# Kernel tuning notes

Hardware: AMD Instinct MI355X
Metric: run time of the kernel (lower is better)

The kernel has to match this reference:

```python
import jax, jax.numpy as jnp
import numpy as np

B, F, D = 2048, 40, 32
CIN = (64, 64)


def _glorot(key, shape):
    fan_in, fan_out = shape[1] * shape[2], shape[0] * shape[2]
    std = jnp.sqrt(2.0 / (fan_in + fan_out)).astype(jnp.float32)
    return jax.random.normal(key, shape, dtype=jnp.float32) * std


def setup_inputs() -> dict:
    key = jax.random.key(0)
    kx, k0, k1 = jax.random.split(key, 3)
    x = jax.random.normal(kx, (B, F, D), dtype=jnp.float32)
    W0 = _glorot(k0, (CIN[0], F * F, D))
    b0 = jnp.zeros((CIN[0],), dtype=jnp.float32)
    W1 = _glorot(k1, (CIN[1], F * CIN[0], D))
    b1 = jnp.zeros((CIN[1],), dtype=jnp.float32)
    return {"x": x, "W0": W0, "b0": b0, "W1": W1, "b1": b1}


def _cin_step(x0, xk, W, b):
    # x0: (B,F,D)  xk: (B,H,D)  W: (O, H*F, D)  b: (O,)
    Bn, H, Dn = xk.shape
    Fn = x0.shape[1]
    # outer product per embedding channel, h-major flatten as in tf.reshape
    z = jnp.einsum('bhd,bfd->bhfd', xk, x0).reshape(Bn, H * Fn, Dn)
    # per-embedding-channel contraction against weights: (B,D,O)
    y = jnp.einsum('bhd,ohd->bdo', z, W) + b
    y = jax.nn.relu(y)
    return jnp.transpose(y, (0, 2, 1))  # (B,O,D)


def reference(x, W0, b0, W1, b1):
    x1 = _cin_step(x, x, W0, b0)
    x2 = _cin_step(x, x1, W1, b1)
    final = jnp.concatenate([x, x1, x2], axis=1)  # (B, F+O0+O1, D)
    return jnp.sum(final, axis=-1)  # (B, F+O0+O1)
```

## Files before the change

### kernel.cpp

```cpp
#include <hip/hip_runtime.h>

typedef unsigned int   u32;
typedef unsigned short u16;
typedef _Float16       f16;

using f16x8  = __attribute__((ext_vector_type(8)))  _Float16;
using f16x4  = __attribute__((ext_vector_type(4)))  _Float16;
using f32x16 = __attribute__((ext_vector_type(16))) float;

#define LLDS16(G, L) __builtin_amdgcn_global_load_lds( \
  (const __attribute__((address_space(1))) u32*)(G), \
  (__attribute__((address_space(3))) u32*)(L), 16, 0, 0)

#define WAITV(N) { asm volatile("s_waitcnt vmcnt(" #N ")" ::: "memory"); \
                   __builtin_amdgcn_sched_barrier(0); }
#define FENCE_BAR() { asm volatile("s_waitcnt lgkmcnt(0)" ::: "memory"); \
                      __builtin_amdgcn_sched_barrier(0); \
                      __builtin_amdgcn_s_barrier(); \
                      __builtin_amdgcn_sched_barrier(0); }
#define BAR() { __builtin_amdgcn_s_barrier(); __builtin_amdgcn_sched_barrier(0); }
#define KEEP(x) asm volatile("" : "+v"(x))

__global__ __launch_bounds__(256)
void prep(const float* __restrict__ x,
          const float* __restrict__ W0, const float* __restrict__ W1,
          f16* __restrict__ xt, f16* __restrict__ W0p, f16* __restrict__ W1p,
          float* __restrict__ out){
  __shared__ char shm[33920];
  const int tid = threadIdx.x;
  if (blockIdx.x < 2560){
    float (*tile)[33] = (float(*)[33])shm;
    const int r0 = blockIdx.x << 5;
    const int c  = tid & 31;
    const int rp = tid >> 5;
#pragma unroll
    for (int p = 0; p < 4; ++p){
      const int r = (p << 3) + rp;
      float v = x[(size_t)(r0 + r) * 32 + c];
      tile[r][c] = v;
      float s = v;
#pragma unroll
      for (int off = 16; off > 0; off >>= 1) s += __shfl_xor(s, off, 32);
      if (c == 0){
        const int row = r0 + r;
        out[(size_t)(row / 40) * 168 + (row % 40)] = s;
      }
    }
    __syncthreads();
#pragma unroll
    for (int p = 0; p < 4; ++p){
      const int dd = (p << 3) + rp;
      xt[(size_t)dd * 81920 + r0 + c] = (f16)tile[c][dd];
    }
  } else {
    u16* t = (u16*)shm;
    int kb = blockIdx.x - 2560;
    const float* in; f16* outp; int K;
    if (kb < 200){ in = W0; outp = W0p; K = 1600; }
    else         { kb -= 200; in = W1; outp = W1p; K = 2560; }
    const int kbase = kb << 3;
#pragma unroll 4
    for (int i = 0; i < 64; ++i){
      const int idx = tid + (i << 8);
      const int o   = idx >> 8;
      const int rem = idx & 255;
      const int e   = rem >> 5;
      const int dd  = rem & 31;
      const float v = in[(size_t)o * (K * 32) + (size_t)(kbase + e) * 32 + dd];
      union { f16 h; u16 u; } cv; cv.h = (f16)v;
      t[dd * 530 + o * 8 + e] = cv.u;
    }
    __syncthreads();
    const u32* t32 = (const u32*)t;
    u32* o32 = (u32*)outp;
    const int obase = kb << 8;
#pragma unroll 4
    for (int i = 0; i < 32; ++i){
      const int idx = tid + (i << 8);
      const int dd  = idx >> 8;
      const int rem = idx & 255;
      o32[(size_t)dd * (K * 32) + obase + rem] = t32[dd * 265 + rem];
    }
  }
}

__global__ __launch_bounds__(256, 2)
void cin_fused(const f16* __restrict__ xt,
               const f16* __restrict__ W0p,
               const f16* __restrict__ W1p,
               const float* __restrict__ b0v, const float* __restrict__ b1v,
               f16* __restrict__ x1s,
               f16* __restrict__ y2s){
  constexpr int X0OFF = 40960;
  constexpr int X1OFF = 53248;
  constexpr int X0MS  = 32 * 96;
  constexpr int X1MS  = 32 * 144;

  const int bid = blockIdx.x;
  const int d   = ((bid & 7) << 2) | ((bid >> 3) & 3);
  const int b0  = (bid >> 5) << 7;
  const int tid = threadIdx.x;
  const int wv  = tid >> 6;
  const int wr  = wv >> 1;
  const int wc  = wv & 1;
  const int l   = tid & 63;
  const int hi  = l >> 5;
  const int lr  = l & 31;

  __shared__ char smem[71680];

  const f16* gW0 = W0p + (size_t)d * 102400;
  const f16* gW1 = W1p + (size_t)d * 163840;

#define ISSUE(I) do { \
    const f16* src_ = ((I) < 10) ? (gW0 + (size_t)(I) * 10240) \
                                 : (gW1 + (size_t)((I) - 10) * 10240); \
    const f16* gt_ = src_ + wv * 2560 + l * 8; \
    char* lb_ = smem + ((I) & 1) * 20480 + wv * 5120; \
    _Pragma("unroll") \
    for (int j_ = 0; j_ < 5; ++j_) LLDS16(gt_ + j_ * 512, lb_ + j_ * 1024); \
  } while (0)

  ISSUE(0);
  ISSUE(1);

  {
    const uint4* src = (const uint4*)(xt + (size_t)d * 81920 + (size_t)b0 * 40);
#pragma unroll
    for (int it = 0; it < 3; ++it){
      const int idx = tid + (it << 8);
      if (idx < 640){
        const int r = idx / 5, c = idx - r * 5;
        *(uint4*)(smem + X0OFF + r * 96 + c * 16) = src[idx];
      }
    }
  }
  __syncthreads();

  const char* x0r = smem + X0OFF + ((wr << 6) + lr) * 96;
  const char* x1r = smem + X1OFF + ((wr << 6) + lr) * 144;
  const int   col = (wc << 5) + lr;
  const float bv1 = b0v[col];
  const float bv2 = b1v[col];

  f16x8 sl[2][5];
#pragma unroll
  for (int m = 0; m < 2; ++m){
    const char* xe = x0r + m * X0MS + hi * 16;
#pragma unroll
    for (int t = 0; t < 4; ++t) sl[m][t] = *(const f16x8*)(xe + t * 16);
    sl[m][4] = *(const f16x8*)(x0r + m * X0MS + (hi ? 0 : 64));
  }
  KEEP(sl[0][0]); KEEP(sl[0][1]); KEEP(sl[0][2]); KEEP(sl[0][3]); KEEP(sl[0][4]);
  KEEP(sl[1][0]); KEEP(sl[1][1]); KEEP(sl[1][2]); KEEP(sl[1][3]); KEEP(sl[1][4]);

  f32x16 acc0 = {0,0,0,0,0,0,0,0,0,0,0,0,0,0,0,0};
  f32x16 acc1 = {0,0,0,0,0,0,0,0,0,0,0,0,0,0,0,0};

  const int vb = (hi << 10) + (wc << 9) + (lr << 4);

  static constexpr int J0[5]  = {0, 4, 3, 2, 1};
  static constexpr int H0[5]  = {0, 0, 1, 2, 3};
  static constexpr int H0b[5] = {0, 1, 1, 2, 3};
  static constexpr int S0[5]  = {0, 1, 0, 0, 0};
  static constexpr int J2[5]  = {2, 1, 0, 4, 3};
  static constexpr int H2[5]  = {0, 1, 2, 2, 3};
  static constexpr int H2b[5] = {0, 1, 2, 3, 3};
  static constexpr int S2[5]  = {0, 0, 0, 1, 0};

#define COMP(BB) do { \
  __builtin_amdgcn_s_setprio(1); \
  _Pragma("unroll") \
  for (int si = 0; si < 5; ++si){ \
    const f16x8 bf0 = *(const f16x8*)((BB) + vb + (si * 4) * 1024); \
    const f16x8 bf2 = *(const f16x8*)((BB) + vb + (si * 4 + 2) * 1024); \
    const f16 xa00 = (S0[si] && hi) ? xh0[H0b[si]] : xh0[H0[si]]; \
    const f16 xa01 = (S0[si] && hi) ? xh1[H0b[si]] : xh1[H0[si]]; \
    const f16 xa20 = (S2[si] && hi) ? xh0[H2b[si]] : xh0[H2[si]]; \
    const f16 xa21 = (S2[si] && hi) ? xh1[H2b[si]] : xh1[H2[si]]; \
    acc0 = __builtin_amdgcn_mfma_f32_32x32x16_f16(sl[0][J0[si]] * xa00, bf0, acc0, 0, 0, 0); \
    acc1 = __builtin_amdgcn_mfma_f32_32x32x16_f16(sl[1][J0[si]] * xa01, bf0, acc1, 0, 0, 0); \
    acc0 = __builtin_amdgcn_mfma_f32_32x32x16_f16(sl[0][J2[si]] * xa20, bf2, acc0, 0, 0, 0); \
    acc1 = __builtin_amdgcn_mfma_f32_32x32x16_f16(sl[1][J2[si]] * xa21, bf2, acc1, 0, 0, 0); \
  } \
  __builtin_amdgcn_s_setprio(0); \
} while (0)

  {
    f16x4 xh0 = *(const f16x4*)(x0r);
    f16x4 xh1 = *(const f16x4*)(x0r + X0MS);
    for (int t = 0; t < 10; ++t){
      const char* bb = smem + (t & 1) * 20480;
      const f16x4 xhn0 = *(const f16x4*)(x0r + (t + 1) * 8);
      const f16x4 xhn1 = *(const f16x4*)(x0r + X0MS + (t + 1) * 8);
      COMP(bb);
      FENCE_BAR();
      ISSUE(t + 2);
      WAITV(5);
      BAR();
      xh0 = xhn0; xh1 = xhn1;
    }
  }

  {
    u16* x1w = (u16*)(smem + X1OFF);
#pragma unroll
    for (int m = 0; m < 2; ++m)
#pragma unroll
      for (int reg = 0; reg < 16; ++reg){
        const int row = (wr << 6) + (m << 5) + (reg & 3) + ((reg >> 2) << 3) + (hi << 2);
        float v = (m ? acc1[reg] : acc0[reg]) + bv1;
        v = v > 0.f ? v : 0.f;
        union { f16 h; u16 u; } cv; cv.h = (f16)v;
        x1w[row * 72 + col] = cv.u;
      }
    const f32x16 fz = {0,0,0,0,0,0,0,0,0,0,0,0,0,0,0,0};
    acc0 = fz; acc1 = fz;
    asm volatile("s_waitcnt lgkmcnt(0)" ::: "memory");
    __builtin_amdgcn_sched_barrier(0);
    WAITV(0);
    BAR();
#pragma unroll
    for (int it = 0; it < 4; ++it){
      const int u   = tid + (it << 8);
      const int row = u >> 3, ch = u & 7;
      const f16x8 vv = *(const f16x8*)((const char*)x1w + row * 144 + ch * 16);
      *(f16x8*)(x1s + (size_t)(b0 + row) * 2048 + d * 64 + ch * 8) = vv;
    }
  }

  {
    f16x4 xh0 = *(const f16x4*)(x1r);
    f16x4 xh1 = *(const f16x4*)(x1r + X1MS);
    for (int t = 0; t < 16; ++t){
      const char* bb = smem + (t & 1) * 20480;
      const f16x4 xhn0 = *(const f16x4*)(x1r + (t + 1) * 8);
      const f16x4 xhn1 = *(const f16x4*)(x1r + X1MS + (t + 1) * 8);
      COMP(bb);
      FENCE_BAR();
      if (t + 2 < 16){
        ISSUE(12 + t);
        WAITV(5);
      } else {
        WAITV(0);
      }
      BAR();
      xh0 = xhn0; xh1 = xhn1;
    }
  }

  {
    u16* yw = (u16*)(smem + X1OFF);
#pragma unroll
    for (int m = 0; m < 2; ++m)
#pragma unroll
      for (int reg = 0; reg < 16; ++reg){
        const int row = (wr << 6) + (m << 5) + (reg & 3) + ((reg >> 2) << 3) + (hi << 2);
        float v = (m ? acc1[reg] : acc0[reg]) + bv2;
        v = v > 0.f ? v : 0.f;
        union { f16 h; u16 u; } cv; cv.h = (f16)v;
        yw[row * 72 + col] = cv.u;
      }
    asm volatile("s_waitcnt lgkmcnt(0)" ::: "memory");
    __builtin_amdgcn_sched_barrier(0);
    BAR();
#pragma unroll
    for (int it = 0; it < 4; ++it){
      const int u   = tid + (it << 8);
      const int row = u >> 3, ch = u & 7;
      const f16x8 vv = *(const f16x8*)((const char*)yw + row * 144 + ch * 16);
      *(f16x8*)(y2s + (size_t)(b0 + row) * 2048 + d * 64 + ch * 8) = vv;
    }
  }
#undef ISSUE
#undef COMP
}

__global__ __launch_bounds__(128)
void finalize(const f16* __restrict__ x1s, const f16* __restrict__ y2s,
              float* __restrict__ out){
  const int b = blockIdx.x;
  const int t = threadIdx.x;
  if (t < 64){
    float s = 0.f;
#pragma unroll
    for (int d = 0; d < 32; ++d) s += (float)x1s[(size_t)b * 2048 + d * 64 + t];
    out[(size_t)b * 168 + 40 + t] = s;
  } else {
    const int o = t - 64;
    float s = 0.f;
#pragma unroll
    for (int d = 0; d < 32; ++d) s += (float)y2s[(size_t)b * 2048 + d * 64 + o];
    out[(size_t)b * 168 + 104 + o] = s;
  }
}

extern "C" void kernel_launch(void* const* d_in, const int* in_sizes, int n_in,
                              void* d_out, int out_size, void* d_ws, size_t ws_size,
                              hipStream_t stream){
  const float* x   = (const float*)d_in[0];
  const float* W0  = (const float*)d_in[1];
  const float* b0v = (const float*)d_in[2];
  const float* W1  = (const float*)d_in[3];
  const float* b1v = (const float*)d_in[4];
  float* out = (float*)d_out;

  char* ws = (char*)d_ws;
  f16* xt  = (f16*)(ws + 0);
  f16* W0p = (f16*)(ws + 5242880);
  f16* W1p = (f16*)(ws + 11796480);
  f16* x1s = (f16*)(ws + 22282240);
  f16* y2s = (f16*)(ws + 30670848);

  prep<<<3080, 256, 0, stream>>>(x, W0, W1, xt, W0p, W1p, out);
  cin_fused<<<512, 256, 0, stream>>>(xt, W0p, W1p, b0v, b1v, x1s, y2s);
  finalize<<<2048, 128, 0, stream>>>(x1s, y2s, out);
}
```

Before: 59.80 us.

## Split CIN fused kernel across 8 waves with one accumulator each

```diff
diff --git a/kernel.cpp b/kernel.cpp
--- a/kernel.cpp
+++ b/kernel.cpp
@@ -84,30 +84,27 @@
   }
 }
 
-__global__ __launch_bounds__(256, 2)
+__global__ __launch_bounds__(512, 4)
 void cin_fused(const f16* __restrict__ xt,
                const f16* __restrict__ W0p,
                const f16* __restrict__ W1p,
                const float* __restrict__ b0v, const float* __restrict__ b1v,
                f16* __restrict__ x1s,
                f16* __restrict__ y2s){
-  constexpr int X0OFF = 40960;
-  constexpr int X1OFF = 53248;
-  constexpr int X0MS  = 32 * 96;
-  constexpr int X1MS  = 32 * 144;
+  constexpr int XOFF = 40960;
 
   const int bid = blockIdx.x;
   const int d   = ((bid & 7) << 2) | ((bid >> 3) & 3);
   const int b0  = (bid >> 5) << 7;
   const int tid = threadIdx.x;
   const int wv  = tid >> 6;
-  const int wr  = wv >> 1;
+  const int rg  = wv >> 1;
   const int wc  = wv & 1;
   const int l   = tid & 63;
   const int hi  = l >> 5;
   const int lr  = l & 31;
 
-  __shared__ char smem[71680];
+  __shared__ char smem[59392];
 
   const f16* gW0 = W0p + (size_t)d * 102400;
   const f16* gW1 = W1p + (size_t)d * 163840;
@@ -115,11 +112,13 @@
 #define ISSUE(I) do { \
     const f16* src_ = ((I) < 10) ? (gW0 + (size_t)(I) * 10240) \
                                  : (gW1 + (size_t)((I) - 10) * 10240); \
-    const f16* gt_ = src_ + wv * 2560 + l * 8; \
-    char* lb_ = smem + ((I) & 1) * 20480 + wv * 5120; \
-    _Pragma("unroll") \
-    for (int j_ = 0; j_ < 5; ++j_) LLDS16(gt_ + j_ * 512, lb_ + j_ * 1024); \
+    const f16* gt_ = src_ + l * 8; \
+    char* lb_ = smem + ((I) & 1) * 20480; \
+    LLDS16(gt_ + (size_t)wv * 512,       lb_ + wv * 1024); \
+    LLDS16(gt_ + (size_t)(8 + wv) * 512, lb_ + (8 + wv) * 1024); \
+    if (wv < 4) LLDS16(gt_ + (size_t)(16 + wv) * 512, lb_ + (16 + wv) * 1024); \
   } while (0)
+#define WAITVP() { if (wv < 4) { WAITV(3); } else { WAITV(2); } }
 
   ISSUE(0);
   ISSUE(1);
@@ -127,35 +126,32 @@
   {
     const uint4* src = (const uint4*)(xt + (size_t)d * 81920 + (size_t)b0 * 40);
 #pragma unroll
-    for (int it = 0; it < 3; ++it){
-      const int idx = tid + (it << 8);
+    for (int it = 0; it < 2; ++it){
+      const int idx = tid + (it << 9);
       if (idx < 640){
         const int r = idx / 5, c = idx - r * 5;
-        *(uint4*)(smem + X0OFF + r * 96 + c * 16) = src[idx];
+        *(uint4*)(smem + XOFF + r * 96 + c * 16) = src[idx];
       }
     }
   }
   __syncthreads();
 
-  const char* x0r = smem + X0OFF + ((wr << 6) + lr) * 96;
-  const char* x1r = smem + X1OFF + ((wr << 6) + lr) * 144;
+  const char* x0r = smem + XOFF + ((rg << 5) + lr) * 96;
+  const char* x1r = smem + XOFF + ((rg << 5) + lr) * 144;
   const int   col = (wc << 5) + lr;
   const float bv1 = b0v[col];
   const float bv2 = b1v[col];
 
-  f16x8 sl[2][5];
-#pragma unroll
-  for (int m = 0; m < 2; ++m){
-    const char* xe = x0r + m * X0MS + hi * 16;
-#pragma unroll
-    for (int t = 0; t < 4; ++t) sl[m][t] = *(const f16x8*)(xe + t * 16);
-    sl[m][4] = *(const f16x8*)(x0r + m * X0MS + (hi ? 0 : 64));
-  }
-  KEEP(sl[0][0]); KEEP(sl[0][1]); KEEP(sl[0][2]); KEEP(sl[0][3]); KEEP(sl[0][4]);
-  KEEP(sl[1][0]); KEEP(sl[1][1]); KEEP(sl[1][2]); KEEP(sl[1][3]); KEEP(sl[1][4]);
-
-  f32x16 acc0 = {0,0,0,0,0,0,0,0,0,0,0,0,0,0,0,0};
-  f32x16 acc1 = {0,0,0,0,0,0,0,0,0,0,0,0,0,0,0,0};
+  f16x8 sl[5];
+  {
+    const char* xe = x0r + hi * 16;
+#pragma unroll
+    for (int t = 0; t < 4; ++t) sl[t] = *(const f16x8*)(xe + t * 16);
+    sl[4] = *(const f16x8*)(x0r + (hi ? 0 : 64));
+  }
+  KEEP(sl[0]); KEEP(sl[1]); KEEP(sl[2]); KEEP(sl[3]); KEEP(sl[4]);
+
+  f32x16 acc = {0,0,0,0,0,0,0,0,0,0,0,0,0,0,0,0};
 
   const int vb = (hi << 10) + (wc << 9) + (lr << 4);
 
@@ -172,57 +168,47 @@
   __builtin_amdgcn_s_setprio(1); \
   _Pragma("unroll") \
   for (int si = 0; si < 5; ++si){ \
-    const f16x8 bf0 = *(const f16x8*)((BB) + vb + (si * 4) * 1024); \
-    const f16x8 bf2 = *(const f16x8*)((BB) + vb + (si * 4 + 2) * 1024); \
-    const f16 xa00 = (S0[si] && hi) ? xh0[H0b[si]] : xh0[H0[si]]; \
-    const f16 xa01 = (S0[si] && hi) ? xh1[H0b[si]] : xh1[H0[si]]; \
-    const f16 xa20 = (S2[si] && hi) ? xh0[H2b[si]] : xh0[H2[si]]; \
-    const f16 xa21 = (S2[si] && hi) ? xh1[H2b[si]] : xh1[H2[si]]; \
-    acc0 = __builtin_amdgcn_mfma_f32_32x32x16_f16(sl[0][J0[si]] * xa00, bf0, acc0, 0, 0, 0); \
-    acc1 = __builtin_amdgcn_mfma_f32_32x32x16_f16(sl[1][J0[si]] * xa01, bf0, acc1, 0, 0, 0); \
-    acc0 = __builtin_amdgcn_mfma_f32_32x32x16_f16(sl[0][J2[si]] * xa20, bf2, acc0, 0, 0, 0); \
-    acc1 = __builtin_amdgcn_mfma_f32_32x32x16_f16(sl[1][J2[si]] * xa21, bf2, acc1, 0, 0, 0); \
+    const f16x8 bf0 = *(const f16x8*)((BB) + vb + si * 4096); \
+    const f16x8 bf2 = *(const f16x8*)((BB) + vb + si * 4096 + 2048); \
+    const f16 xa0 = (S0[si] && hi) ? xh[H0b[si]] : xh[H0[si]]; \
+    const f16 xa2 = (S2[si] && hi) ? xh[H2b[si]] : xh[H2[si]]; \
+    acc = __builtin_amdgcn_mfma_f32_32x32x16_f16(sl[J0[si]] * xa0, bf0, acc, 0, 0, 0); \
+    acc = __builtin_amdgcn_mfma_f32_32x32x16_f16(sl[J2[si]] * xa2, bf2, acc, 0, 0, 0); \
   } \
   __builtin_amdgcn_s_setprio(0); \
 } while (0)
 
   {
-    f16x4 xh0 = *(const f16x4*)(x0r);
-    f16x4 xh1 = *(const f16x4*)(x0r + X0MS);
+    f16x4 xh = *(const f16x4*)(x0r);
     for (int t = 0; t < 10; ++t){
       const char* bb = smem + (t & 1) * 20480;
-      const f16x4 xhn0 = *(const f16x4*)(x0r + (t + 1) * 8);
-      const f16x4 xhn1 = *(const f16x4*)(x0r + X0MS + (t + 1) * 8);
+      const f16x4 xhn = *(const f16x4*)(x0r + (t + 1) * 8);
       COMP(bb);
       FENCE_BAR();
       ISSUE(t + 2);
-      WAITV(5);
+      WAITVP();
       BAR();
-      xh0 = xhn0; xh1 = xhn1;
-    }
-  }
-
-  {
-    u16* x1w = (u16*)(smem + X1OFF);
-#pragma unroll
-    for (int m = 0; m < 2; ++m)
-#pragma unroll
-      for (int reg = 0; reg < 16; ++reg){
-        const int row = (wr << 6) + (m << 5) + (reg & 3) + ((reg >> 2) << 3) + (hi << 2);
-        float v = (m ? acc1[reg] : acc0[reg]) + bv1;
-        v = v > 0.f ? v : 0.f;
-        union { f16 h; u16 u; } cv; cv.h = (f16)v;
-        x1w[row * 72 + col] = cv.u;
-      }
-    const f32x16 fz = {0,0,0,0,0,0,0,0,0,0,0,0,0,0,0,0};
-    acc0 = fz; acc1 = fz;
+      xh = xhn;
+    }
+  }
+
+  {
+    u16* x1w = (u16*)(smem + XOFF);
+#pragma unroll
+    for (int reg = 0; reg < 16; ++reg){
+      const int row = (rg << 5) + (reg & 3) + ((reg >> 2) << 3) + (hi << 2);
+      float v = acc[reg] + bv1;
+      v = v > 0.f ? v : 0.f;
+      union { f16 h; u16 u; } cv; cv.h = (f16)v;
+      x1w[row * 72 + col] = cv.u;
+      acc[reg] = 0.f;
+    }
     asm volatile("s_waitcnt lgkmcnt(0)" ::: "memory");
     __builtin_amdgcn_sched_barrier(0);
-    WAITV(0);
     BAR();
 #pragma unroll
-    for (int it = 0; it < 4; ++it){
-      const int u   = tid + (it << 8);
+    for (int it = 0; it < 2; ++it){
+      const int u   = tid + (it << 9);
       const int row = u >> 3, ch = u & 7;
       const f16x8 vv = *(const f16x8*)((const char*)x1w + row * 144 + ch * 16);
       *(f16x8*)(x1s + (size_t)(b0 + row) * 2048 + d * 64 + ch * 8) = vv;
@@ -230,49 +216,46 @@
   }
 
   {
-    f16x4 xh0 = *(const f16x4*)(x1r);
-    f16x4 xh1 = *(const f16x4*)(x1r + X1MS);
+    f16x4 xh = *(const f16x4*)(x1r);
     for (int t = 0; t < 16; ++t){
       const char* bb = smem + (t & 1) * 20480;
-      const f16x4 xhn0 = *(const f16x4*)(x1r + (t + 1) * 8);
-      const f16x4 xhn1 = *(const f16x4*)(x1r + X1MS + (t + 1) * 8);
+      const f16x4 xhn = *(const f16x4*)(x1r + (t + 1) * 8);
       COMP(bb);
       FENCE_BAR();
       if (t + 2 < 16){
         ISSUE(12 + t);
-        WAITV(5);
+        WAITVP();
       } else {
         WAITV(0);
       }
       BAR();
-      xh0 = xhn0; xh1 = xhn1;
-    }
-  }
-
-  {
-    u16* yw = (u16*)(smem + X1OFF);
-#pragma unroll
-    for (int m = 0; m < 2; ++m)
-#pragma unroll
-      for (int reg = 0; reg < 16; ++reg){
-        const int row = (wr << 6) + (m << 5) + (reg & 3) + ((reg >> 2) << 3) + (hi << 2);
-        float v = (m ? acc1[reg] : acc0[reg]) + bv2;
-        v = v > 0.f ? v : 0.f;
-        union { f16 h; u16 u; } cv; cv.h = (f16)v;
-        yw[row * 72 + col] = cv.u;
-      }
+      xh = xhn;
+    }
+  }
+
+  {
+    u16* yw = (u16*)(smem + XOFF);
+#pragma unroll
+    for (int reg = 0; reg < 16; ++reg){
+      const int row = (rg << 5) + (reg & 3) + ((reg >> 2) << 3) + (hi << 2);
+      float v = acc[reg] + bv2;
+      v = v > 0.f ? v : 0.f;
+      union { f16 h; u16 u; } cv; cv.h = (f16)v;
+      yw[row * 72 + col] = cv.u;
+    }
     asm volatile("s_waitcnt lgkmcnt(0)" ::: "memory");
     __builtin_amdgcn_sched_barrier(0);
     BAR();
 #pragma unroll
-    for (int it = 0; it < 4; ++it){
-      const int u   = tid + (it << 8);
+    for (int it = 0; it < 2; ++it){
+      const int u   = tid + (it << 9);
       const int row = u >> 3, ch = u & 7;
       const f16x8 vv = *(const f16x8*)((const char*)yw + row * 144 + ch * 16);
       *(f16x8*)(y2s + (size_t)(b0 + row) * 2048 + d * 64 + ch * 8) = vv;
     }
   }
 #undef ISSUE
+#undef WAITVP
 #undef COMP
 }
 
@@ -313,6 +296,6 @@
   f16* y2s = (f16*)(ws + 30670848);
 
   prep<<<3080, 256, 0, stream>>>(x, W0, W1, xt, W0p, W1p, out);
-  cin_fused<<<512, 256, 0, stream>>>(xt, W0p, W1p, b0v, b1v, x1s, y2s);
+  cin_fused<<<512, 512, 0, stream>>>(xt, W0p, W1p, b0v, b1v, x1s, y2s);
   finalize<<<2048, 128, 0, stream>>>(x1s, y2s, out);
 }
```

Result: no change. 60.22 us (+0.7%).

## Triple-buffer weight staging with one barrier per step and split MFMA accumulators

Applied to the files above, without the earlier changes.

```diff
diff --git a/kernel.cpp b/kernel.cpp
--- a/kernel.cpp
+++ b/kernel.cpp
@@ -91,10 +91,9 @@
                const float* __restrict__ b0v, const float* __restrict__ b1v,
                f16* __restrict__ x1s,
                f16* __restrict__ y2s){
-  constexpr int X0OFF = 40960;
-  constexpr int X1OFF = 53248;
-  constexpr int X0MS  = 32 * 96;
-  constexpr int X1MS  = 32 * 144;
+  constexpr int XOFF = 61440;
+  constexpr int X0MS = 32 * 96;
+  constexpr int X1MS = 32 * 144;
 
   const int bid = blockIdx.x;
   const int d   = ((bid & 7) << 2) | ((bid >> 3) & 3);
@@ -107,22 +106,23 @@
   const int hi  = l >> 5;
   const int lr  = l & 31;
 
-  __shared__ char smem[71680];
+  __shared__ char smem[79872];
 
   const f16* gW0 = W0p + (size_t)d * 102400;
   const f16* gW1 = W1p + (size_t)d * 163840;
 
-#define ISSUE(I) do { \
+#define ISSUE(I, BUF) do { \
     const f16* src_ = ((I) < 10) ? (gW0 + (size_t)(I) * 10240) \
                                  : (gW1 + (size_t)((I) - 10) * 10240); \
-    const f16* gt_ = src_ + wv * 2560 + l * 8; \
-    char* lb_ = smem + ((I) & 1) * 20480 + wv * 5120; \
+    const f16* gt_ = src_ + l * 8; \
+    char* lb_ = smem + (BUF) * 20480; \
     _Pragma("unroll") \
-    for (int j_ = 0; j_ < 5; ++j_) LLDS16(gt_ + j_ * 512, lb_ + j_ * 1024); \
+    for (int j_ = 0; j_ < 5; ++j_) \
+      LLDS16(gt_ + (size_t)(wv + 4 * j_) * 512, lb_ + (wv + 4 * j_) * 1024); \
   } while (0)
 
-  ISSUE(0);
-  ISSUE(1);
+  ISSUE(0, 0);
+  ISSUE(1, 1);
 
   {
     const uint4* src = (const uint4*)(xt + (size_t)d * 81920 + (size_t)b0 * 40);
@@ -131,14 +131,14 @@
       const int idx = tid + (it << 8);
       if (idx < 640){
         const int r = idx / 5, c = idx - r * 5;
-        *(uint4*)(smem + X0OFF + r * 96 + c * 16) = src[idx];
+        *(uint4*)(smem + XOFF + r * 96 + c * 16) = src[idx];
       }
     }
   }
   __syncthreads();
 
-  const char* x0r = smem + X0OFF + ((wr << 6) + lr) * 96;
-  const char* x1r = smem + X1OFF + ((wr << 6) + lr) * 144;
+  const char* x0r = smem + XOFF + ((wr << 6) + lr) * 96;
+  const char* x1r = smem + XOFF + ((wr << 6) + lr) * 144;
   const int   col = (wc << 5) + lr;
   const float bv1 = b0v[col];
   const float bv2 = b1v[col];
@@ -154,8 +154,8 @@
   KEEP(sl[0][0]); KEEP(sl[0][1]); KEEP(sl[0][2]); KEEP(sl[0][3]); KEEP(sl[0][4]);
   KEEP(sl[1][0]); KEEP(sl[1][1]); KEEP(sl[1][2]); KEEP(sl[1][3]); KEEP(sl[1][4]);
 
-  f32x16 acc0 = {0,0,0,0,0,0,0,0,0,0,0,0,0,0,0,0};
-  f32x16 acc1 = {0,0,0,0,0,0,0,0,0,0,0,0,0,0,0,0};
+  const f32x16 fz = {0,0,0,0,0,0,0,0,0,0,0,0,0,0,0,0};
+  f32x16 acc0a = fz, acc0b = fz, acc1a = fz, acc1b = fz;
 
   const int vb = (hi << 10) + (wc << 9) + (lr << 4);
 
@@ -172,54 +172,47 @@
   __builtin_amdgcn_s_setprio(1); \
   _Pragma("unroll") \
   for (int si = 0; si < 5; ++si){ \
-    const f16x8 bf0 = *(const f16x8*)((BB) + vb + (si * 4) * 1024); \
-    const f16x8 bf2 = *(const f16x8*)((BB) + vb + (si * 4 + 2) * 1024); \
+    const f16x8 bf0 = *(const f16x8*)((BB) + vb + si * 4096); \
+    const f16x8 bf2 = *(const f16x8*)((BB) + vb + si * 4096 + 2048); \
     const f16 xa00 = (S0[si] && hi) ? xh0[H0b[si]] : xh0[H0[si]]; \
     const f16 xa01 = (S0[si] && hi) ? xh1[H0b[si]] : xh1[H0[si]]; \
     const f16 xa20 = (S2[si] && hi) ? xh0[H2b[si]] : xh0[H2[si]]; \
     const f16 xa21 = (S2[si] && hi) ? xh1[H2b[si]] : xh1[H2[si]]; \
-    acc0 = __builtin_amdgcn_mfma_f32_32x32x16_f16(sl[0][J0[si]] * xa00, bf0, acc0, 0, 0, 0); \
-    acc1 = __builtin_amdgcn_mfma_f32_32x32x16_f16(sl[1][J0[si]] * xa01, bf0, acc1, 0, 0, 0); \
-    acc0 = __builtin_amdgcn_mfma_f32_32x32x16_f16(sl[0][J2[si]] * xa20, bf2, acc0, 0, 0, 0); \
-    acc1 = __builtin_amdgcn_mfma_f32_32x32x16_f16(sl[1][J2[si]] * xa21, bf2, acc1, 0, 0, 0); \
+    acc0a = __builtin_amdgcn_mfma_f32_32x32x16_f16(sl[0][J0[si]] * xa00, bf0, acc0a, 0, 0, 0); \
+    acc1a = __builtin_amdgcn_mfma_f32_32x32x16_f16(sl[1][J0[si]] * xa01, bf0, acc1a, 0, 0, 0); \
+    acc0b = __builtin_amdgcn_mfma_f32_32x32x16_f16(sl[0][J2[si]] * xa20, bf2, acc0b, 0, 0, 0); \
+    acc1b = __builtin_amdgcn_mfma_f32_32x32x16_f16(sl[1][J2[si]] * xa21, bf2, acc1b, 0, 0, 0); \
   } \
   __builtin_amdgcn_s_setprio(0); \
 } while (0)
 
+  int cur = 0, ib = 2;
+
+  for (int t = 0; t < 10; ++t){
+    if (t > 0){ WAITV(5); BAR(); }
+    ISSUE(t + 2, ib);
+    const f16x4 xh0 = *(const f16x4*)(x0r + t * 8);
+    const f16x4 xh1 = *(const f16x4*)(x0r + X0MS + t * 8);
+    COMP(smem + cur * 20480);
+    cur = cur + 1; if (cur == 3) cur = 0;
+    ib  = ib + 1;  if (ib == 3)  ib = 0;
+  }
+
   {
-    f16x4 xh0 = *(const f16x4*)(x0r);
-    f16x4 xh1 = *(const f16x4*)(x0r + X0MS);
-    for (int t = 0; t < 10; ++t){
-      const char* bb = smem + (t & 1) * 20480;
-      const f16x4 xhn0 = *(const f16x4*)(x0r + (t + 1) * 8);
-      const f16x4 xhn1 = *(const f16x4*)(x0r + X0MS + (t + 1) * 8);
-      COMP(bb);
-      FENCE_BAR();
-      ISSUE(t + 2);
-      WAITV(5);
-      BAR();
-      xh0 = xhn0; xh1 = xhn1;
-    }
-  }
-
-  {
-    u16* x1w = (u16*)(smem + X1OFF);
+    FENCE_BAR();
+    u16* x1w = (u16*)(smem + XOFF);
 #pragma unroll
     for (int m = 0; m < 2; ++m)
 #pragma unroll
       for (int reg = 0; reg < 16; ++reg){
         const int row = (wr << 6) + (m << 5) + (reg & 3) + ((reg >> 2) << 3) + (hi << 2);
-        float v = (m ? acc1[reg] : acc0[reg]) + bv1;
+        float v = (m ? acc1a[reg] + acc1b[reg] : acc0a[reg] + acc0b[reg]) + bv1;
         v = v > 0.f ? v : 0.f;
         union { f16 h; u16 u; } cv; cv.h = (f16)v;
         x1w[row * 72 + col] = cv.u;
       }
-    const f32x16 fz = {0,0,0,0,0,0,0,0,0,0,0,0,0,0,0,0};
-    acc0 = fz; acc1 = fz;
-    asm volatile("s_waitcnt lgkmcnt(0)" ::: "memory");
-    __builtin_amdgcn_sched_barrier(0);
-    WAITV(0);
-    BAR();
+    acc0a = fz; acc0b = fz; acc1a = fz; acc1b = fz;
+    FENCE_BAR();
 #pragma unroll
     for (int it = 0; it < 4; ++it){
       const int u   = tid + (it << 8);
@@ -229,41 +222,33 @@
     }
   }
 
+  for (int t2 = 0; t2 < 16; ++t2){
+    if (t2 < 2)       { WAITV(9); }
+    else if (t2 < 15) { WAITV(5); }
+    else              { WAITV(0); }
+    BAR();
+    if (t2 + 2 < 16) ISSUE(12 + t2, ib);
+    const f16x4 xh0 = *(const f16x4*)(x1r + t2 * 8);
+    const f16x4 xh1 = *(const f16x4*)(x1r + X1MS + t2 * 8);
+    COMP(smem + cur * 20480);
+    cur = cur + 1; if (cur == 3) cur = 0;
+    ib  = ib + 1;  if (ib == 3)  ib = 0;
+  }
+
   {
-    f16x4 xh0 = *(const f16x4*)(x1r);
-    f16x4 xh1 = *(const f16x4*)(x1r + X1MS);
-    for (int t = 0; t < 16; ++t){
-      const char* bb = smem + (t & 1) * 20480;
-      const f16x4 xhn0 = *(const f16x4*)(x1r + (t + 1) * 8);
-      const f16x4 xhn1 = *(const f16x4*)(x1r + X1MS + (t + 1) * 8);
-      COMP(bb);
-      FENCE_BAR();
-      if (t + 2 < 16){
-        ISSUE(12 + t);
-        WAITV(5);
-      } else {
-        WAITV(0);
-      }
-      BAR();
-      xh0 = xhn0; xh1 = xhn1;
-    }
-  }
-
-  {
-    u16* yw = (u16*)(smem + X1OFF);
+    FENCE_BAR();
+    u16* yw = (u16*)(smem + XOFF);
 #pragma unroll
     for (int m = 0; m < 2; ++m)
 #pragma unroll
       for (int reg = 0; reg < 16; ++reg){
         const int row = (wr << 6) + (m << 5) + (reg & 3) + ((reg >> 2) << 3) + (hi << 2);
-        float v = (m ? acc1[reg] : acc0[reg]) + bv2;
+        float v = (m ? acc1a[reg] + acc1b[reg] : acc0a[reg] + acc0b[reg]) + bv2;
         v = v > 0.f ? v : 0.f;
         union { f16 h; u16 u; } cv; cv.h = (f16)v;
         yw[row * 72 + col] = cv.u;
       }
-    asm volatile("s_waitcnt lgkmcnt(0)" ::: "memory");
-    __builtin_amdgcn_sched_barrier(0);
-    BAR();
+    FENCE_BAR();
 #pragma unroll
     for (int it = 0; it < 4; ++it){
       const int u   = tid + (it << 8);
```

Result: no change. 60.43 us (+1.1%).
